# Optimization experiments

Hardware: AMD Instinct MI355X
Metric: run time of the kernel (lower is better)

## Reference

```python
import jax, jax.numpy as jnp
import numpy as np

ALPHA = 1.0
EPS = 1e-8

def setup_inputs() -> dict:
    key = jax.random.key(0)
    k1, k2, k3 = jax.random.split(key, 3)
    B, L, S, H, E, D = 4, 2048, 2048, 8, 64, 64
    queries = jax.random.normal(k1, (B, L, H, E), dtype=jnp.float32)
    keys = jax.random.normal(k2, (B, S, H, E), dtype=jnp.float32)
    values = jax.random.normal(k3, (B, S, H, D), dtype=jnp.float32)
    return {"queries": queries, "keys": keys, "values": values}

def reference(queries, keys, values):
    E = queries.shape[3]
    scale = 1.0 / jnp.sqrt(jnp.asarray(E, queries.dtype))
    # dot_product: [B,H,L,S]
    dot = jnp.einsum('blhe,bshe->bhls', queries, keys)
    q_norm2 = jnp.sum(queries ** 2, axis=-1).transpose(0, 2, 1)[..., :, None]  # [B,H,L,1]
    k_norm2 = jnp.sum(keys ** 2, axis=-1).transpose(0, 2, 1)[..., None, :]     # [B,H,1,S]
    wedge2 = jax.nn.relu(q_norm2 * k_norm2 - dot ** 2)
    wedge = jnp.sqrt(wedge2 + EPS)
    scores = ((1.0 - ALPHA) * dot + ALPHA * wedge) * scale
    A = jax.nn.softmax(scores, axis=-1)  # dropout in eval mode = identity
    out = jnp.einsum('bhls,bshd->blhd', A, values)
    return out
```

## Files before the change

kernel.cpp:

```cpp
#include <hip/hip_runtime.h>

typedef __attribute__((ext_vector_type(2))) float f32x2;
typedef __attribute__((ext_vector_type(4))) float f32x4;
typedef __attribute__((ext_vector_type(4))) float float4v;
typedef __attribute__((ext_vector_type(8))) short bf16x8;
typedef __attribute__((ext_vector_type(8))) unsigned short ushort8;

#define DEVI static __device__ __forceinline__

namespace {
constexpr int kL = 2048, kS = 2048, kH = 8;
constexpr int QB = 64, KVB = 64, NKT = kS / KVB;
constexpr float kC = 0.18033688f;
constexpr int TILE = 8192;
constexpr int BH = 32 * TILE;
constexpr int LBUF = 2 * TILE;
}

DEVI int swz(int byteoff) { return byteoff ^ (((byteoff >> 7) & 7) << 4); }

DEVI unsigned cvtpk(float lo, float hi) {
  unsigned r;
  asm("v_cvt_pk_bf16_f32 %0, %1, %2" : "=v"(r) : "v"(lo), "v"(hi));
  return r;
}

DEVI f32x2 pkmul(f32x2 a, f32x2 b) {
  f32x2 r;
  asm("v_pk_mul_f32 %0, %1, %2" : "=v"(r) : "v"(a), "v"(b));
  return r;
}

__global__ __launch_bounds__(256) void prep_k(const float* __restrict__ Kg,
                                              char* __restrict__ Kb,
                                              float* __restrict__ kn2g) {
  const int chunk = (int)blockIdx.x * 256 + (int)threadIdx.x;
  const int tile = chunk >> 9;
  const int i = chunk & 511;
  const int bh = tile >> 5, kt = tile & 31;
  const int b = bh >> 3, h = bh & 7;
  const int row = i >> 3;
  const int colsel = (i & 7) ^ (row & 7);
  const int s = kt * 64 + row;
  const float* src = Kg + (((size_t)b * kS + s) * kH + h) * 64 + colsel * 8;
  float4v v0 = *(const float4v*)(src);
  float4v v1 = *(const float4v*)(src + 4);
  float pn = v0.x*v0.x + v0.y*v0.y + v0.z*v0.z + v0.w*v0.w
           + v1.x*v1.x + v1.y*v1.y + v1.z*v1.z + v1.w*v1.w;
  union { unsigned w[4]; ushort8 u; } o;
  o.w[0] = cvtpk(v0.x, v0.y); o.w[1] = cvtpk(v0.z, v0.w);
  o.w[2] = cvtpk(v1.x, v1.y); o.w[3] = cvtpk(v1.z, v1.w);
  *(ushort8*)(Kb + (size_t)tile * TILE + i * 16) = o.u;
  pn += __shfl_xor(pn, 1);
  pn += __shfl_xor(pn, 2);
  pn += __shfl_xor(pn, 4);
  if ((i & 7) == 0) kn2g[tile * 64 + row] = pn;
}

__global__ __launch_bounds__(256) void prep_v(const float* __restrict__ Vg,
                                              char* __restrict__ Vt) {
  __shared__ char tile[64 * 128];
  const int t = (int)threadIdx.x;
  const int bid = (int)blockIdx.x;
  const int st = bid & 31, bh = bid >> 5;
  const int b = bh >> 3, h = bh & 7;
  {
    const int sl = t >> 2, c0 = (t & 3) * 16;
    const float* src = Vg + (((size_t)b * kS + st * 64 + sl) * kH + h) * 64 + c0;
    float4v v0 = *(const float4v*)(src);
    float4v v1 = *(const float4v*)(src + 4);
    float4v v2 = *(const float4v*)(src + 8);
    float4v v3 = *(const float4v*)(src + 12);
    union { unsigned w[4]; ushort8 u; } t0, t1;
    t0.w[0] = cvtpk(v0.x, v0.y); t0.w[1] = cvtpk(v0.z, v0.w);
    t0.w[2] = cvtpk(v1.x, v1.y); t0.w[3] = cvtpk(v1.z, v1.w);
    t1.w[0] = cvtpk(v2.x, v2.y); t1.w[1] = cvtpk(v2.z, v2.w);
    t1.w[2] = cvtpk(v3.x, v3.y); t1.w[3] = cvtpk(v3.z, v3.w);
    *(ushort8*)(tile + swz(sl * 128 + c0 * 2)) = t0.u;
    *(ushort8*)(tile + swz(sl * 128 + c0 * 2 + 16)) = t1.u;
  }
  __syncthreads();
  char* dst = Vt + (size_t)bid * TILE;
#pragma unroll
  for (int cc = 0; cc < 2; ++cc) {
    const int i = t * 2 + cc;
    const int z = swz(i * 16);
    const int d = z >> 7;
    const int k0 = ((z >> 4) & 7) * 8;
    union { unsigned short s[8]; ushort8 u; } o;
#pragma unroll
    for (int j = 0; j < 8; ++j) {
      const int k = k0 + j;
      const int sig = (((k >> 5) * 2 + ((k & 7) >> 2)) << 4) |
                      (((k >> 3) & 3) << 2) | (k & 3);
      o.s[j] = *(const unsigned short*)(tile + swz(sig * 128 + d * 2));
    }
    *(ushort8*)(dst + i * 16) = o.u;
  }
}

__global__ __launch_bounds__(256, 4) void geo_attn_kernel(
    const float* __restrict__ Qg, const char* __restrict__ Kb,
    const char* __restrict__ Vt, const float* __restrict__ kn2g,
    float* __restrict__ Og) {
  __shared__ char lds[2 * LBUF];

  const int t = (int)threadIdx.x;
  const int wv = t >> 6, lane = t & 63, gg = lane >> 4, cl = lane & 15;
  const int n = (int)blockIdx.x;
  const int bh = (n & 7) * 4 + ((n >> 3) & 3);
  const int l0 = (n >> 5) * QB;
  const int b = bh >> 3, h = bh & 7;

  const int q = l0 + wv * 16 + cl;
  const float* qp = Qg + (((size_t)b * kL + q) * kH + h) * 64;
  float4v x0 = *(const float4v*)(qp + gg * 8);
  float4v x1 = *(const float4v*)(qp + gg * 8 + 4);
  float4v x2 = *(const float4v*)(qp + gg * 8 + 32);
  float4v x3 = *(const float4v*)(qp + gg * 8 + 36);
  x0 *= kC; x1 *= kC; x2 *= kC; x3 *= kC;
  float pn = 0.f;
#pragma unroll
  for (int j = 0; j < 4; ++j) {
    pn = fmaf(x0[j], x0[j], pn); pn = fmaf(x1[j], x1[j], pn);
    pn = fmaf(x2[j], x2[j], pn); pn = fmaf(x3[j], x3[j], pn);
  }
  union frag { bf16x8 v; unsigned w[4]; };
  frag qb0, qb1;
  qb0.w[0] = cvtpk(x0.x, x0.y); qb0.w[1] = cvtpk(x0.z, x0.w);
  qb0.w[2] = cvtpk(x1.x, x1.y); qb0.w[3] = cvtpk(x1.z, x1.w);
  qb1.w[0] = cvtpk(x2.x, x2.y); qb1.w[1] = cvtpk(x2.z, x2.w);
  qb1.w[2] = cvtpk(x3.x, x3.y); qb1.w[3] = cvtpk(x3.z, x3.w);
  pn += __shfl_xor(pn, 16);
  pn += __shfl_xor(pn, 32);
  const f32x2 qn2d = {pn, pn};

  frag vone;
  vone.w[0] = vone.w[1] = vone.w[2] = vone.w[3] = 0x3F803F80u;

  const char* pA = lds + ((cl * 128 + gg * 16) ^ ((cl & 7) << 4));
  const char* pB = lds + ((cl * 128 + gg * 16 + 64) ^ ((cl & 7) << 4));

  const bool isK = (wv < 2);
  const char* gp = (isK ? Kb : Vt) + (size_t)bh * BH + (wv & 1) * 4096 + lane * 16;
  const int ldsoff = (isK ? 0 : TILE) + (wv & 1) * 4096;
  char* const sd0 = lds + ldsoff;
  char* const sd1 = lds + LBUF + ldsoff;
  const float* kn2p = kn2g + bh * 2048 + gg * 4;

#define STAGE(SD) do { \
    __builtin_amdgcn_global_load_lds((__attribute__((address_space(1))) void*)(gp),        (__attribute__((address_space(3))) void*)(SD),        16, 0, 0); \
    __builtin_amdgcn_global_load_lds((__attribute__((address_space(1))) void*)(gp + 1024), (__attribute__((address_space(3))) void*)((SD) + 1024), 16, 0, 0); \
    __builtin_amdgcn_global_load_lds((__attribute__((address_space(1))) void*)(gp + 2048), (__attribute__((address_space(3))) void*)((SD) + 2048), 16, 0, 0); \
    __builtin_amdgcn_global_load_lds((__attribute__((address_space(1))) void*)(gp + 3072), (__attribute__((address_space(3))) void*)((SD) + 3072), 16, 0, 0); \
    gp += TILE; \
  } while (0)

  f32x4 oacc[4];
#pragma unroll
  for (int dt = 0; dt < 4; ++dt) oacc[dt] = (f32x4){0.f, 0.f, 0.f, 0.f};
  f32x4 lacc = (f32x4){0.f, 0.f, 0.f, 0.f};

#define BODY(BO, KF) do { \
    float4v kn2v[4]; \
    _Pragma("unroll") for (int nt = 0; nt < 4; ++nt) \
      kn2v[nt] = *(const float4v*)(kn2p + (KF) + nt * 16); \
    f32x4 dacc[4]; \
    __builtin_amdgcn_s_setprio(1); \
    _Pragma("unroll") for (int nt = 0; nt < 4; ++nt) { \
      bf16x8 ka0 = *(const bf16x8*)(pA + (BO) + nt * 2048); \
      bf16x8 ka1 = *(const bf16x8*)(pB + (BO) + nt * 2048); \
      f32x4 acc = {0.f, 0.f, 0.f, 0.f}; \
      acc = __builtin_amdgcn_mfma_f32_16x16x32_bf16(ka0, qb0.v, acc, 0, 0, 0); \
      acc = __builtin_amdgcn_mfma_f32_16x16x32_bf16(ka1, qb1.v, acc, 0, 0, 0); \
      dacc[nt] = acc; } \
    __builtin_amdgcn_s_setprio(0); \
    f32x2 qk2lo[4], qk2hi[4]; \
    _Pragma("unroll") for (int nt = 0; nt < 4; ++nt) { \
      const f32x2 klo = {kn2v[nt][0], kn2v[nt][1]}; \
      const f32x2 khi = {kn2v[nt][2], kn2v[nt][3]}; \
      qk2lo[nt] = pkmul(qn2d, klo); \
      qk2hi[nt] = pkmul(qn2d, khi); } \
    bf16x8 vb0[4], vb1[4]; \
    _Pragma("unroll") for (int dt = 0; dt < 4; ++dt) { \
      vb0[dt] = *(const bf16x8*)(pA + (BO) + TILE + dt * 2048); \
      vb1[dt] = *(const bf16x8*)(pB + (BO) + TILE + dt * 2048); } \
    float sc[4][4]; \
    _Pragma("unroll") for (int nt = 0; nt < 2; ++nt) \
      _Pragma("unroll") for (int r = 0; r < 4; ++r) { \
        const float d = dacc[nt][r]; \
        const float qk2 = (r < 2) ? qk2lo[nt][r] : qk2hi[nt][r - 2]; \
        const float w2 = fmaf(-d, d, qk2); \
        sc[nt][r] = __builtin_amdgcn_exp2f(__builtin_amdgcn_sqrtf(fabsf(w2))); } \
    frag pa0; \
    pa0.w[0] = cvtpk(sc[0][0], sc[0][1]); pa0.w[1] = cvtpk(sc[0][2], sc[0][3]); \
    pa0.w[2] = cvtpk(sc[1][0], sc[1][1]); pa0.w[3] = cvtpk(sc[1][2], sc[1][3]); \
    __builtin_amdgcn_s_setprio(1); \
    _Pragma("unroll") for (int dt = 0; dt < 4; ++dt) \
      oacc[dt] = __builtin_amdgcn_mfma_f32_16x16x32_bf16(pa0.v, vb0[dt], oacc[dt], 0, 0, 0); \
    lacc = __builtin_amdgcn_mfma_f32_16x16x32_bf16(pa0.v, vone.v, lacc, 0, 0, 0); \
    __builtin_amdgcn_s_setprio(0); \
    _Pragma("unroll") for (int nt = 2; nt < 4; ++nt) \
      _Pragma("unroll") for (int r = 0; r < 4; ++r) { \
        const float d = dacc[nt][r]; \
        const float qk2 = (r < 2) ? qk2lo[nt][r] : qk2hi[nt][r - 2]; \
        const float w2 = fmaf(-d, d, qk2); \
        sc[nt][r] = __builtin_amdgcn_exp2f(__builtin_amdgcn_sqrtf(fabsf(w2))); } \
    frag pa1; \
    pa1.w[0] = cvtpk(sc[2][0], sc[2][1]); pa1.w[1] = cvtpk(sc[2][2], sc[2][3]); \
    pa1.w[2] = cvtpk(sc[3][0], sc[3][1]); pa1.w[3] = cvtpk(sc[3][2], sc[3][3]); \
    __builtin_amdgcn_s_setprio(1); \
    _Pragma("unroll") for (int dt = 0; dt < 4; ++dt) \
      oacc[dt] = __builtin_amdgcn_mfma_f32_16x16x32_bf16(pa1.v, vb1[dt], oacc[dt], 0, 0, 0); \
    lacc = __builtin_amdgcn_mfma_f32_16x16x32_bf16(pa1.v, vone.v, lacc, 0, 0, 0); \
    __builtin_amdgcn_s_setprio(0); \
  } while (0)

  STAGE(sd0);
  __syncthreads();

#pragma unroll 1
  for (int it = 0; it < NKT / 2; ++it) {
    STAGE(sd1);
    BODY(0, 0);
    __syncthreads();
    STAGE(sd0);
    BODY(LBUF, 64);
    __syncthreads();
    kn2p += 128;
  }
#undef STAGE
#undef BODY

#pragma unroll
  for (int r = 0; r < 4; ++r) {
    const int l = l0 + wv * 16 + gg * 4 + r;
    const float inv = 1.f / lacc[r];
    float* op = Og + (((size_t)b * kL + l) * kH + h) * 64;
#pragma unroll
    for (int dt = 0; dt < 4; ++dt)
      op[dt * 16 + cl] = oacc[dt][r] * inv;
  }
}

extern "C" void kernel_launch(void* const* d_in, const int* in_sizes, int n_in,
                              void* d_out, int out_size, void* d_ws, size_t ws_size,
                              hipStream_t stream) {
  const float* Qg = (const float*)d_in[0];
  const float* Kg = (const float*)d_in[1];
  const float* Vg = (const float*)d_in[2];
  float* Og = (float*)d_out;
  char* Kb = (char*)d_ws;
  char* Vt = (char*)d_ws + ((size_t)8 << 20);
  float* kn2g = (float*)((char*)d_ws + ((size_t)16 << 20));
  prep_k<<<2048, 256, 0, stream>>>(Kg, Kb, kn2g);
  prep_v<<<1024, 256, 0, stream>>>(Vg, Vt);
  geo_attn_kernel<<<dim3(1024), dim3(256), 0, stream>>>(Qg, Kb, Vt, kn2g, Og);
}
```

Before: 71.80 us.

## Process two query sub-tiles per wave to double K/V tile reuse

Each wave now handles 32 query rows, as two 16-row sub-tiles, instead of 16. The query block grows to 128 and the grid is halved to 512 blocks. Each K/V tile staged in LDS, together with its V fragments and key norms, is reused by both sub-tiles, which halves global-to-LDS traffic and LDS fragment reads per unit of work. In exchange, register pressure roughly doubles for accumulators and Q fragments, launch bounds drop to 2 blocks per SM, and there are fewer blocks to fill the 256 CUs.

```diff
diff --git a/kernel.cpp b/kernel.cpp
--- a/kernel.cpp
+++ b/kernel.cpp
@@ -10,7 +10,7 @@
 
 namespace {
 constexpr int kL = 2048, kS = 2048, kH = 8;
-constexpr int QB = 64, KVB = 64, NKT = kS / KVB;
+constexpr int QB = 128, NKT = 32;
 constexpr float kC = 0.18033688f;
 constexpr int TILE = 8192;
 constexpr int BH = 32 * TILE;
@@ -99,7 +99,7 @@
   }
 }
 
-__global__ __launch_bounds__(256, 4) void geo_attn_kernel(
+__global__ __launch_bounds__(256, 2) void geo_attn_kernel(
     const float* __restrict__ Qg, const char* __restrict__ Kb,
     const char* __restrict__ Vt, const float* __restrict__ kn2g,
     float* __restrict__ Og) {
@@ -112,28 +112,53 @@
   const int l0 = (n >> 5) * QB;
   const int b = bh >> 3, h = bh & 7;
 
-  const int q = l0 + wv * 16 + cl;
-  const float* qp = Qg + (((size_t)b * kL + q) * kH + h) * 64;
-  float4v x0 = *(const float4v*)(qp + gg * 8);
-  float4v x1 = *(const float4v*)(qp + gg * 8 + 4);
-  float4v x2 = *(const float4v*)(qp + gg * 8 + 32);
-  float4v x3 = *(const float4v*)(qp + gg * 8 + 36);
-  x0 *= kC; x1 *= kC; x2 *= kC; x3 *= kC;
-  float pn = 0.f;
-#pragma unroll
-  for (int j = 0; j < 4; ++j) {
-    pn = fmaf(x0[j], x0[j], pn); pn = fmaf(x1[j], x1[j], pn);
-    pn = fmaf(x2[j], x2[j], pn); pn = fmaf(x3[j], x3[j], pn);
-  }
   union frag { bf16x8 v; unsigned w[4]; };
-  frag qb0, qb1;
-  qb0.w[0] = cvtpk(x0.x, x0.y); qb0.w[1] = cvtpk(x0.z, x0.w);
-  qb0.w[2] = cvtpk(x1.x, x1.y); qb0.w[3] = cvtpk(x1.z, x1.w);
-  qb1.w[0] = cvtpk(x2.x, x2.y); qb1.w[1] = cvtpk(x2.z, x2.w);
-  qb1.w[2] = cvtpk(x3.x, x3.y); qb1.w[3] = cvtpk(x3.z, x3.w);
-  pn += __shfl_xor(pn, 16);
-  pn += __shfl_xor(pn, 32);
-  const f32x2 qn2d = {pn, pn};
+
+  const int qA = l0 + wv * 32 + cl;
+  const float* qpA = Qg + (((size_t)b * kL + qA) * kH + h) * 64;
+  const float* qpB = qpA + 16 * kH * 64;
+  frag qbA0, qbA1, qbB0, qbB1;
+  f32x2 qn2dA, qn2dB;
+  {
+    float4v x0 = *(const float4v*)(qpA + gg * 8);
+    float4v x1 = *(const float4v*)(qpA + gg * 8 + 4);
+    float4v x2 = *(const float4v*)(qpA + gg * 8 + 32);
+    float4v x3 = *(const float4v*)(qpA + gg * 8 + 36);
+    x0 *= kC; x1 *= kC; x2 *= kC; x3 *= kC;
+    float pn = 0.f;
+#pragma unroll
+    for (int j = 0; j < 4; ++j) {
+      pn = fmaf(x0[j], x0[j], pn); pn = fmaf(x1[j], x1[j], pn);
+      pn = fmaf(x2[j], x2[j], pn); pn = fmaf(x3[j], x3[j], pn);
+    }
+    qbA0.w[0] = cvtpk(x0.x, x0.y); qbA0.w[1] = cvtpk(x0.z, x0.w);
+    qbA0.w[2] = cvtpk(x1.x, x1.y); qbA0.w[3] = cvtpk(x1.z, x1.w);
+    qbA1.w[0] = cvtpk(x2.x, x2.y); qbA1.w[1] = cvtpk(x2.z, x2.w);
+    qbA1.w[2] = cvtpk(x3.x, x3.y); qbA1.w[3] = cvtpk(x3.z, x3.w);
+    pn += __shfl_xor(pn, 16);
+    pn += __shfl_xor(pn, 32);
+    qn2dA = (f32x2){pn, pn};
+  }
+  {
+    float4v x0 = *(const float4v*)(qpB + gg * 8);
+    float4v x1 = *(const float4v*)(qpB + gg * 8 + 4);
+    float4v x2 = *(const float4v*)(qpB + gg * 8 + 32);
+    float4v x3 = *(const float4v*)(qpB + gg * 8 + 36);
+    x0 *= kC; x1 *= kC; x2 *= kC; x3 *= kC;
+    float pn = 0.f;
+#pragma unroll
+    for (int j = 0; j < 4; ++j) {
+      pn = fmaf(x0[j], x0[j], pn); pn = fmaf(x1[j], x1[j], pn);
+      pn = fmaf(x2[j], x2[j], pn); pn = fmaf(x3[j], x3[j], pn);
+    }
+    qbB0.w[0] = cvtpk(x0.x, x0.y); qbB0.w[1] = cvtpk(x0.z, x0.w);
+    qbB0.w[2] = cvtpk(x1.x, x1.y); qbB0.w[3] = cvtpk(x1.z, x1.w);
+    qbB1.w[0] = cvtpk(x2.x, x2.y); qbB1.w[1] = cvtpk(x2.z, x2.w);
+    qbB1.w[2] = cvtpk(x3.x, x3.y); qbB1.w[3] = cvtpk(x3.z, x3.w);
+    pn += __shfl_xor(pn, 16);
+    pn += __shfl_xor(pn, 32);
+    qn2dB = (f32x2){pn, pn};
+  }
 
   frag vone;
   vone.w[0] = vone.w[1] = vone.w[2] = vone.w[3] = 0x3F803F80u;
@@ -156,35 +181,31 @@
     gp += TILE; \
   } while (0)
 
-  f32x4 oacc[4];
-#pragma unroll
-  for (int dt = 0; dt < 4; ++dt) oacc[dt] = (f32x4){0.f, 0.f, 0.f, 0.f};
-  f32x4 lacc = (f32x4){0.f, 0.f, 0.f, 0.f};
-
-#define BODY(BO, KF) do { \
-    float4v kn2v[4]; \
-    _Pragma("unroll") for (int nt = 0; nt < 4; ++nt) \
-      kn2v[nt] = *(const float4v*)(kn2p + (KF) + nt * 16); \
+  f32x4 oaccA[4], oaccB[4];
+#pragma unroll
+  for (int dt = 0; dt < 4; ++dt) {
+    oaccA[dt] = (f32x4){0.f, 0.f, 0.f, 0.f};
+    oaccB[dt] = (f32x4){0.f, 0.f, 0.f, 0.f};
+  }
+  f32x4 laccA = (f32x4){0.f, 0.f, 0.f, 0.f};
+  f32x4 laccB = (f32x4){0.f, 0.f, 0.f, 0.f};
+
+#define HBODY(BO, Q0, Q1, QN2D, OACC, LACC) do { \
     f32x4 dacc[4]; \
     __builtin_amdgcn_s_setprio(1); \
     _Pragma("unroll") for (int nt = 0; nt < 4; ++nt) { \
       bf16x8 ka0 = *(const bf16x8*)(pA + (BO) + nt * 2048); \
       bf16x8 ka1 = *(const bf16x8*)(pB + (BO) + nt * 2048); \
       f32x4 acc = {0.f, 0.f, 0.f, 0.f}; \
-      acc = __builtin_amdgcn_mfma_f32_16x16x32_bf16(ka0, qb0.v, acc, 0, 0, 0); \
-      acc = __builtin_amdgcn_mfma_f32_16x16x32_bf16(ka1, qb1.v, acc, 0, 0, 0); \
-      dacc[nt] = acc; } \
+      acc = __builtin_amdgcn_mfma_f32_16x16x32_bf16(ka0, (Q0).v, acc, 0, 0, 0); \
+      dacc[nt] = __builtin_amdgcn_mfma_f32_16x16x32_bf16(ka1, (Q1).v, acc, 0, 0, 0); } \
     __builtin_amdgcn_s_setprio(0); \
     f32x2 qk2lo[4], qk2hi[4]; \
     _Pragma("unroll") for (int nt = 0; nt < 4; ++nt) { \
       const f32x2 klo = {kn2v[nt][0], kn2v[nt][1]}; \
       const f32x2 khi = {kn2v[nt][2], kn2v[nt][3]}; \
-      qk2lo[nt] = pkmul(qn2d, klo); \
-      qk2hi[nt] = pkmul(qn2d, khi); } \
-    bf16x8 vb0[4], vb1[4]; \
-    _Pragma("unroll") for (int dt = 0; dt < 4; ++dt) { \
-      vb0[dt] = *(const bf16x8*)(pA + (BO) + TILE + dt * 2048); \
-      vb1[dt] = *(const bf16x8*)(pB + (BO) + TILE + dt * 2048); } \
+      qk2lo[nt] = pkmul(QN2D, klo); \
+      qk2hi[nt] = pkmul(QN2D, khi); } \
     float sc[4][4]; \
     _Pragma("unroll") for (int nt = 0; nt < 2; ++nt) \
       _Pragma("unroll") for (int r = 0; r < 4; ++r) { \
@@ -197,8 +218,8 @@
     pa0.w[2] = cvtpk(sc[1][0], sc[1][1]); pa0.w[3] = cvtpk(sc[1][2], sc[1][3]); \
     __builtin_amdgcn_s_setprio(1); \
     _Pragma("unroll") for (int dt = 0; dt < 4; ++dt) \
-      oacc[dt] = __builtin_amdgcn_mfma_f32_16x16x32_bf16(pa0.v, vb0[dt], oacc[dt], 0, 0, 0); \
-    lacc = __builtin_amdgcn_mfma_f32_16x16x32_bf16(pa0.v, vone.v, lacc, 0, 0, 0); \
+      OACC[dt] = __builtin_amdgcn_mfma_f32_16x16x32_bf16(pa0.v, vb0[dt], OACC[dt], 0, 0, 0); \
+    LACC = __builtin_amdgcn_mfma_f32_16x16x32_bf16(pa0.v, vone.v, LACC, 0, 0, 0); \
     __builtin_amdgcn_s_setprio(0); \
     _Pragma("unroll") for (int nt = 2; nt < 4; ++nt) \
       _Pragma("unroll") for (int r = 0; r < 4; ++r) { \
@@ -211,9 +232,21 @@
     pa1.w[2] = cvtpk(sc[3][0], sc[3][1]); pa1.w[3] = cvtpk(sc[3][2], sc[3][3]); \
     __builtin_amdgcn_s_setprio(1); \
     _Pragma("unroll") for (int dt = 0; dt < 4; ++dt) \
-      oacc[dt] = __builtin_amdgcn_mfma_f32_16x16x32_bf16(pa1.v, vb1[dt], oacc[dt], 0, 0, 0); \
-    lacc = __builtin_amdgcn_mfma_f32_16x16x32_bf16(pa1.v, vone.v, lacc, 0, 0, 0); \
+      OACC[dt] = __builtin_amdgcn_mfma_f32_16x16x32_bf16(pa1.v, vb1[dt], OACC[dt], 0, 0, 0); \
+    LACC = __builtin_amdgcn_mfma_f32_16x16x32_bf16(pa1.v, vone.v, LACC, 0, 0, 0); \
     __builtin_amdgcn_s_setprio(0); \
+  } while (0)
+
+#define BODY(BO, KF) do { \
+    float4v kn2v[4]; \
+    _Pragma("unroll") for (int nt = 0; nt < 4; ++nt) \
+      kn2v[nt] = *(const float4v*)(kn2p + (KF) + nt * 16); \
+    bf16x8 vb0[4], vb1[4]; \
+    _Pragma("unroll") for (int dt = 0; dt < 4; ++dt) { \
+      vb0[dt] = *(const bf16x8*)(pA + (BO) + TILE + dt * 2048); \
+      vb1[dt] = *(const bf16x8*)(pB + (BO) + TILE + dt * 2048); } \
+    HBODY(BO, qbA0, qbA1, qn2dA, oaccA, laccA); \
+    HBODY(BO, qbB0, qbB1, qn2dB, oaccB, laccB); \
   } while (0)
 
   STAGE(sd0);
@@ -231,15 +264,21 @@
   }
 #undef STAGE
 #undef BODY
+#undef HBODY
 
 #pragma unroll
   for (int r = 0; r < 4; ++r) {
-    const int l = l0 + wv * 16 + gg * 4 + r;
-    const float inv = 1.f / lacc[r];
-    float* op = Og + (((size_t)b * kL + l) * kH + h) * 64;
+    const int lA = l0 + wv * 32 + gg * 4 + r;
+    const float invA = 1.f / laccA[r];
+    float* opA = Og + (((size_t)b * kL + lA) * kH + h) * 64;
 #pragma unroll
     for (int dt = 0; dt < 4; ++dt)
-      op[dt * 16 + cl] = oacc[dt][r] * inv;
+      opA[dt * 16 + cl] = oaccA[dt][r] * invA;
+    const float invB = 1.f / laccB[r];
+    float* opB = opA + 16 * kH * 64;
+#pragma unroll
+    for (int dt = 0; dt < 4; ++dt)
+      opB[dt * 16 + cl] = oaccB[dt][r] * invB;
   }
 }
 
@@ -255,5 +294,5 @@
   float* kn2g = (float*)((char*)d_ws + ((size_t)16 << 20));
   prep_k<<<2048, 256, 0, stream>>>(Kg, Kb, kn2g);
   prep_v<<<1024, 256, 0, stream>>>(Vg, Vt);
-  geo_attn_kernel<<<dim3(1024), dim3(256), 0, stream>>>(Qg, Kb, Vt, kn2g, Og);
-}
+  geo_attn_kernel<<<dim3(512), dim3(256), 0, stream>>>(Qg, Kb, Vt, kn2g, Og);
+}
```

After: 71.42 us. No clear change (-0.5%).
